# Optimization experiments

Hardware: AMD Instinct MI355X
Metric: run time of the kernel (lower is better)

Reference implementation:

```python
import jax, jax.numpy as jnp
import numpy as np

T_MAX = 26  # hardcoded 26 char steps in the torch module

def _resize(x, hw):
    # torch F.interpolate bilinear, align_corners=False (half-pixel) == jax linear, no antialias
    return jax.image.resize(x, x.shape[:-2] + hw, method='linear', antialias=False)

def _ce(logits, labels):
    # per-element cross entropy, labels int
    logp = jax.nn.log_softmax(logits, axis=-1)
    return -jnp.take_along_axis(logp, labels[:, None].astype(jnp.int32), axis=-1)[:, 0]


def setup_inputs() -> dict:
    key = jax.random.key(0)
    ks = jax.random.split(key, 6)
    b, H, W, L = 512, 32, 128, 64
    hm, wm, hl, wl = 16, 64, 8, 32
    return {
        'masks': jax.random.uniform(ks[0], (b, 1, H, W), dtype=jnp.float32),
        'backfore_feature': jax.random.normal(ks[1], (b, 2, H, W), dtype=jnp.float32),
        'seq1_attention_map': jax.random.uniform(ks[2], (b, L, T_MAX), dtype=jnp.float32),
        'char_middle': jax.random.normal(ks[3], (b, 27, hm, wm), dtype=jnp.float32),
        'char_low': jax.random.normal(ks[4], (b, 27, hl, wl), dtype=jnp.float32),
        'length': jax.random.randint(ks[5], (b,), 2, 27),
        'iteration': 1000,
        'alpha': jnp.float32(0.1),
    }


def reference(masks, backfore_feature, seq1_attention_map, char_middle, char_low, length, iteration, alpha):
    b, _, H, W = masks.shape
    f32 = masks.dtype
    masks_i = (masks > 0.5).astype(jnp.int32)                      # [b,1,H,W]
    sm = jax.nn.softmax(backfore_feature, axis=1)                  # [b,2,H,W]

    # ---- SegLoss: CE applied to softmax probs as if logits (faithful to torch) ----
    per_elem = _ce(sm.transpose(0, 2, 3, 1).reshape(-1, 2), masks_i.reshape(-1))
    if iteration > 20000:
        value = per_elem.reshape(b, -1).mean(1)
        sel = (value < 1.0).astype(f32)
        predmask_loss = (value * sel).sum() / jnp.maximum(sel.sum(), 1.0)
    else:
        predmask_loss = per_elem.mean()

    fore_mask = (sm[:, 1] > 0.5).astype(jnp.int32)[:, None]        # [b,1,H,W], int -> no grad
    Attn = jnp.transpose(seq1_attention_map, (0, 2, 1))            # [b,26,L]
    n = length - 1                                                  # valid chars per sample
    nf = n.astype(f32)
    row_valid = (jnp.arange(T_MAX)[None, :] < n[:, None]).astype(f32)  # [b,26]

    # ---- Correct_1D_Location (seg mask detached; Attn gets grads) ----
    fore_d = jax.lax.stop_gradient(fore_mask)
    interp = _resize(Attn[:, None], (T_MAX, W))[:, 0]              # [b,26,W]
    # pairwise sum_{i<j} sum_w (v_i v_j)^2 over the first n rows, vectorized
    sq = jnp.square(interp) * row_valid[:, :, None]
    S = sq.sum(1)
    S2 = jnp.square(sq).sum(1)
    irrelevant = (0.5 * (jnp.square(S) - S2).sum(-1) / nf).sum()
    act = jax.nn.sigmoid(70.0 * (interp - 0.1)) * row_valid[:, :, None]
    # sum_t act[t,w] * mask[h,w] == (sum_t act)[w] * mask[h,w]
    char_sum = jnp.clip(act.sum(1)[:, None, :] * fore_d[:, 0].astype(f32), 0.0, 1.0)  # [b,H,W]
    single2 = jnp.stack([1.0 - char_sum, char_sum], axis=-1)       # [b,H,W,2]
    correct_loss = _ce(single2.reshape(-1, 2), fore_d.reshape(-1)).mean() + irrelevant

    # ---- Char_Segmention_Loss (attention and fore mask detached) ----
    attn_clr = jax.lax.stop_gradient(Attn) * row_valid[:, :, None]  # clear_noise

    def char_branch(char_feat):
        h, w = char_feat.shape[2], char_feat.shape[3]
        fm = (_resize(fore_d.astype(f32), (h, w)) >= 0.4).astype(jnp.int32)   # [b,1,h,w]
        ai = _resize(attn_clr[:, None], (T_MAX, w))[:, 0]
        ab = (ai > alpha).astype(jnp.int32)                                   # [b,26,w]
        single = ab[:, :, None, :] * fm                                       # [b,26,h,w]
        mask27 = jnp.concatenate([1 - fm, single], axis=1)                    # [b,27,h,w]
        labels = jnp.argmax(mask27, axis=1).reshape(-1)
        cel = _ce(char_feat.transpose(0, 2, 3, 1).reshape(-1, 27), labels).mean()
        soft = jax.nn.softmax(char_feat, axis=1)
        m1 = soft[:, 1:].reshape(b, T_MAX, -1)
        m2 = mask27[:, 1:].astype(f32).reshape(b, T_MAX, -1)
        inter = (m1 * m2).sum(-1)
        score = (2.0 * inter + 1.0) / (m1.sum(-1) + m2.sum(-1) + 1.0)         # [b,26]
        dice = (((1.0 - score) * row_valid).sum(-1) / nf).sum() / b
        return cel + dice, mask27, soft

    loss_middle, _, soft_mid = char_branch(char_middle)
    loss_low, mask_low, soft_low = char_branch(char_low)

    return (predmask_loss, correct_loss, loss_low, loss_middle,
            mask_low, soft_mid[:, 1:], soft_low[:, 1:])
```

## Files before the change

### kernel.cpp

```cpp
#include <hip/hip_runtime.h>
#include <hip/hip_bf16.h>
#include <math.h>

#define NB 512
#define TT 26
#define LL 64
#define HH 32
#define WW 128

typedef unsigned long long ull;

__device__ __forceinline__ float wave_sum(float v) {
#pragma unroll
  for (int o = 32; o > 0; o >>= 1) v += __shfl_xor(v, o, 64);
  return v;
}

template<int CTRL, int RM>
__device__ __forceinline__ float dpp_add(float x) {
  int y = __builtin_amdgcn_update_dpp(0, __float_as_int(x), CTRL, RM, 0xf, true);
  return x + __int_as_float(y);
}
__device__ __forceinline__ float wave_red63(float x) {
  x = dpp_add<0x111, 0xf>(x);
  x = dpp_add<0x112, 0xf>(x);
  x = dpp_add<0x114, 0xf>(x);
  x = dpp_add<0x118, 0xf>(x);
  x = dpp_add<0x142, 0xa>(x);
  x = dpp_add<0x143, 0xc>(x);
  return x;
}

__global__ __launch_bounds__(128) void k_phase1(
    const float* __restrict__ seq, const int* __restrict__ length,
    const float* __restrict__ alpha_p, float* __restrict__ wsA,
    ull* __restrict__ amid, unsigned int* __restrict__ alow,
    float* __restrict__ irr_part)
{
  int b = blockIdx.x;
  int tid = threadIdx.x;
  __shared__ float att[LL * TT];
  __shared__ float wpart[2];
  const float* sb = seq + (size_t)b * (LL * TT);
  for (int i = tid; i < LL * TT; i += 128) att[i] = sb[i];
  __syncthreads();
  int n = length[b] - 1;
  float alpha = alpha_p[0];

  int w = tid;
  int k = w >> 1;
  int i0, i1; float c0, c1;
  if ((w & 1) == 0) {
    if (k == 0) { i0 = 0; i1 = 0; c0 = 1.f; c1 = 0.f; }
    else        { i0 = k - 1; i1 = k; c0 = 0.25f; c1 = 0.75f; }
  } else {
    if (k == 63) { i0 = 63; i1 = 63; c0 = 1.f; c1 = 0.f; }
    else         { i0 = k; i1 = k + 1; c0 = 0.75f; c1 = 0.25f; }
  }
  float S = 0.f, S2 = 0.f, A = 0.f;
  for (int t = 0; t < n; ++t) {
    float v = c0 * att[i0 * TT + t] + c1 * att[i1 * TT + t];
    float s = v * v;
    S += s; S2 += s * s;
    A += 1.f / (1.f + __expf(-70.f * (v - 0.1f)));
  }
  wsA[b * WW + w] = A;

  float c = S * S - S2;
  c = wave_sum(c);
  if ((tid & 63) == 0) wpart[tid >> 6] = c;
  __syncthreads();
  if (tid == 0) irr_part[b] = 0.5f * (wpart[0] + wpart[1]) / (float)n;

  if (tid < 64) {
    int x = tid;
    for (int t = 0; t < TT; ++t) {
      bool pred = (t < n) && (att[x * TT + t] > alpha);
      ull m = __ballot(pred);
      if (x == 0) amid[b * TT + t] = m;
    }
  } else {
    int x = tid - 64;
    for (int t = 0; t < TT; ++t) {
      bool pred = (x < 32) && (t < n) &&
                  (0.5f * (att[(2 * x) * TT + t] + att[(2 * x + 1) * TT + t]) > alpha);
      ull m = __ballot(pred);
      if (x == 0) alow[b * TT + t] = (unsigned int)m;
    }
  }
}

__global__ __launch_bounds__(256) void k_phase2(
    const float* __restrict__ masks, const float* __restrict__ bf,
    const float* __restrict__ wsA, float* __restrict__ seg_part,
    float* __restrict__ cor_part, ull* __restrict__ fmsk)
{
  int bid = blockIdx.x;
  int b = bid >> 2, q = bid & 3;
  int tid = threadIdx.x;
  int lane = tid & 63, wv = tid >> 6;
  const float* mb = masks + (size_t)b * 4096 + q * 1024;
  const float* fb = bf + (size_t)b * 8192 + q * 1024;

  float A = wsA[b * WW + (tid & 127)];
  float cs = fminf(fmaxf(A, 0.f), 1.f);
  float ce_fore = log1pf(__expf(1.f - 2.f * cs));

  float seg_acc = 0.f, cor_acc = 0.f;
  for (int k = 0; k < 4; ++k) {
    int px = k * 256 + tid;
    float m = mb[px];
    float b0 = fb[px];
    float b1 = fb[4096 + px];
    float mx = fmaxf(b0, b1);
    float e0 = __expf(b0 - mx), e1 = __expf(b1 - mx);
    float inv = 1.f / (e0 + e1);
    float p0 = e0 * inv, p1 = e1 * inv;
    float pm = fmaxf(p0, p1);
    float lse = pm + log1pf(__expf(-fabsf(p1 - p0)));
    seg_acc += lse - ((m > 0.5f) ? p1 : p0);
    bool fore = b1 > b0;
    cor_acc += fore ? ce_fore : 0.313261687518222834f;
    ull fbm = __ballot(fore);
    if (lane == 0) fmsk[(size_t)b * 64 + q * 16 + k * 4 + wv] = fbm;
  }
  seg_acc = wave_sum(seg_acc);
  cor_acc = wave_sum(cor_acc);
  __shared__ float ps[4], pc[4];
  if (lane == 0) { ps[wv] = seg_acc; pc[wv] = cor_acc; }
  __syncthreads();
  if (tid == 0) {
    seg_part[bid] = ps[0] + ps[1] + ps[2] + ps[3];
    cor_part[bid] = pc[0] + pc[1] + pc[2] + pc[3];
  }
}

__global__ __launch_bounds__(512) void k_chars(
    const float* __restrict__ cm, const float* __restrict__ cl,
    const ull* __restrict__ fmsk, const ull* __restrict__ amid,
    const unsigned int* __restrict__ alow,
    float* __restrict__ out_mask, float* __restrict__ out_smid,
    float* __restrict__ out_slow,
    float* __restrict__ celm_part, float* __restrict__ cell_part,
    float* __restrict__ inter_midP, float* __restrict__ m1s_midP, float* __restrict__ m2s_midP,
    float* __restrict__ inter_low, float* __restrict__ m1s_low, float* __restrict__ m2s_low)
{
  int blk = blockIdx.x;
  int tid = threadIdx.x;
  int lane = tid & 63, wv = tid >> 6;

  __shared__ float s_red_in[8][TT], s_red_m1[8][TT], s_ce[8];

  if (blk >= 256) {
    int bm_ = blk - 256;
    int b = bm_ >> 1, h = bm_ & 1;
    int ly = tid >> 6;
    int x = tid & 63;
    int px = h * 512 + tid;
    __shared__ ull s_bits[TT];
    __shared__ unsigned s_cols[64];
    __shared__ ull s_fmw[32];
    __shared__ ull s_fmrow[8];
    if (tid < TT) s_bits[tid] = amid[b * TT + tid];
    if (tid >= 32 && tid < 64) s_fmw[tid - 32] = fmsk[(size_t)b * 64 + h * 32 + (tid - 32)];
    __syncthreads();
    if (tid < 64) {
      unsigned cb = 0;
#pragma unroll
      for (int t = 0; t < TT; ++t) cb |= (unsigned)((s_bits[t] >> tid) & 1ULL) << t;
      s_cols[tid] = cb;
    }
    __syncthreads();

    int word = x >> 5;
    int p = (x & 31) * 2;
    ull r0 = s_fmw[4 * ly + word];
    ull r1 = s_fmw[4 * ly + 2 + word];
    int cnt = (int)((r0 >> p) & 1) + (int)((r0 >> (p + 1)) & 1)
            + (int)((r1 >> p) & 1) + (int)((r1 >> (p + 1)) & 1);
    bool fm = cnt >= 2;
    unsigned cbk = s_cols[x];
    int lab = (fm && cbk) ? __ffs((int)cbk) : 0;
    if (!fm) cbk = 0;
    ull bm = __ballot(fm);
    if (lane == 0) s_fmrow[wv] = bm;

    const float* base = cm + (size_t)b * 27 * 1024 + px;
    float v[27];
    float xl = 0.f, s0 = 0.f;
#pragma unroll
    for (int c = 0; c < 27; ++c) {
      float r = base[(size_t)c * 1024];
      xl = (c == lab) ? r : xl;
      r = __expf(r);
      v[c] = r;
      s0 += r;
    }
    float inv0 = 1.f / s0;
    float ce_part = __logf(s0) - xl;

    float* os = out_smid + (size_t)b * 26 * 1024 + px;
#pragma unroll
    for (int t = 0; t < TT; ++t) {
      float m1 = v[t + 1] * inv0;
      os[(size_t)t * 1024] = m1;
      float ri = wave_red63(((cbk >> t) & 1) ? m1 : 0.f);
      float rm = wave_red63(m1);
      if (lane == 63) { s_red_in[wv][t] = ri; s_red_m1[wv][t] = rm; }
    }
    float rce = wave_red63(ce_part);
    if (lane == 63) s_ce[wv] = rce;
    __syncthreads();
    if (tid < TT) {
      float m2v = 0.f;
#pragma unroll
      for (int r = 0; r < 8; ++r) m2v += (float)__popcll(s_fmrow[r] & s_bits[tid]);
      float si = 0.f, sm = 0.f;
#pragma unroll
      for (int w = 0; w < 8; ++w) { si += s_red_in[w][tid]; sm += s_red_m1[w][tid]; }
      int o = (2 * b + h) * TT + tid;
      m2s_midP[o] = m2v;
      inter_midP[o] = si;
      m1s_midP[o] = sm;
    }
    if (tid == TT) {
      float c8 = 0.f;
#pragma unroll
      for (int w = 0; w < 8; ++w) c8 += s_ce[w];
      celm_part[2 * b + h] = c8;
    }
  } else {
    int blkL = blk;
    int bI = tid >> 8;
    int bb = blkL * 2 + bI;
    int px = tid & 255;
    int y = px >> 5, x = px & 31;
    __shared__ unsigned l_bits[2][TT];
    __shared__ unsigned s_colsL[2][32];
    __shared__ ull s_fmwL[2][64];
    __shared__ unsigned s_fmrow32[2][8];
    if (tid < 2 * TT) {
      int bi = tid / TT, t = tid - bi * TT;
      l_bits[bi][t] = alow[(blkL * 2 + bi) * TT + t];
    }
    if (tid >= 128 && tid < 256) {
      int j = tid - 128;
      s_fmwL[j >> 6][j & 63] = fmsk[(size_t)(blkL * 2 + (j >> 6)) * 64 + (j & 63)];
    }
    __syncthreads();
    if (tid < 64) {
      int bi = tid >> 5, xc = tid & 31;
      unsigned cb = 0;
#pragma unroll
      for (int t = 0; t < TT; ++t) cb |= ((l_bits[bi][t] >> xc) & 1u) << t;
      s_colsL[bi][xc] = cb;
    }
    __syncthreads();

    int wb = 4 * x + 1;
    int word = wb >> 6;
    int p = wb & 63;
    ull r0 = s_fmwL[bI][(4 * y + 1) * 2 + word];
    ull r1 = s_fmwL[bI][(4 * y + 2) * 2 + word];
    int cnt = (int)((r0 >> p) & 1) + (int)((r0 >> (p + 1)) & 1)
            + (int)((r1 >> p) & 1) + (int)((r1 >> (p + 1)) & 1);
    bool fm = cnt >= 2;
    unsigned cbk = s_colsL[bI][x];
    int lab = (fm && cbk) ? __ffs((int)cbk) : 0;
    if (!fm) cbk = 0;
    ull bm = __ballot(fm);
    if (lane == 0) {
      int wq = wv & 3;
      s_fmrow32[bI][2 * wq] = (unsigned)bm;
      s_fmrow32[bI][2 * wq + 1] = (unsigned)(bm >> 32);
    }

    const float* base = cl + (size_t)bb * 27 * 256 + px;
    float v[27];
    float xl = 0.f, s0 = 0.f;
#pragma unroll
    for (int c = 0; c < 27; ++c) {
      float r = base[(size_t)c * 256];
      xl = (c == lab) ? r : xl;
      r = __expf(r);
      v[c] = r;
      s0 += r;
    }
    float inv0 = 1.f / s0;
    float ce_part = __logf(s0) - xl;

    float* om  = out_mask + (size_t)bb * 27 * 256 + px;
    float* osf = out_slow + (size_t)bb * 26 * 256 + px;
    om[0] = fm ? 0.f : 1.f;
#pragma unroll
    for (int t = 0; t < TT; ++t) {
      float m1 = v[t + 1] * inv0;
      osf[(size_t)t * 256] = m1;
      bool m2 = (cbk >> t) & 1;
      om[(size_t)(t + 1) * 256] = m2 ? 1.f : 0.f;
      float ri = wave_red63(m2 ? m1 : 0.f);
      float rm = wave_red63(m1);
      if (lane == 63) { s_red_in[wv][t] = ri; s_red_m1[wv][t] = rm; }
    }
    float rce = wave_red63(ce_part);
    if (lane == 63) s_ce[wv] = rce;
    __syncthreads();
    if (tid < 2 * TT) {
      int bi = tid / TT, t = tid - bi * TT;
      float m2v = 0.f;
#pragma unroll
      for (int r = 0; r < 8; ++r) m2v += (float)__popc(s_fmrow32[bi][r] & l_bits[bi][t]);
      float si = 0.f, sm = 0.f;
#pragma unroll
      for (int w = 0; w < 4; ++w) { si += s_red_in[bi * 4 + w][t]; sm += s_red_m1[bi * 4 + w][t]; }
      int o = (blkL * 2 + bi) * TT + t;
      m2s_low[o] = m2v;
      inter_low[o] = si;
      m1s_low[o] = sm;
    }
    if (tid >= 2 * TT && tid < 2 * TT + 2) {
      int bi = tid - 2 * TT;
      cell_part[blkL * 2 + bi] = s_ce[bi * 4] + s_ce[bi * 4 + 1] + s_ce[bi * 4 + 2] + s_ce[bi * 4 + 3];
    }
  }
}

__global__ __launch_bounds__(1024) void k_final(
    const float* __restrict__ seg_part, const float* __restrict__ cor_part,
    const float* __restrict__ irr_part, const float* __restrict__ celm_part,
    const float* __restrict__ cell_part,
    const float* __restrict__ inter_midP, const float* __restrict__ m1s_midP,
    const float* __restrict__ m2s_midP,
    const float* __restrict__ inter_low, const float* __restrict__ m1s_low,
    const float* __restrict__ m2s_low,
    const int* __restrict__ length, const int* __restrict__ iter_p,
    float* __restrict__ out)
{
  int tid = threadIdx.x;
  float dm = 0.f, dl = 0.f;
  for (int i = tid; i < NB * TT; i += 1024) {
    int b = i / TT, t = i - b * TT;
    int n = length[b] - 1;
    if (t < n) {
      float inv_n = 1.f / (float)n;
      int o0 = (2 * b) * TT + t, o1 = (2 * b + 1) * TT + t;
      float im = inter_midP[o0] + inter_midP[o1];
      float mm = m1s_midP[o0] + m1s_midP[o1];
      float m2 = m2s_midP[o0] + m2s_midP[o1];
      dm += (1.f - (2.f * im + 1.f) / (mm + m2 + 1.f)) * inv_n;
      dl += (1.f - (2.f * inter_low[i] + 1.f) / (m1s_low[i] + m2s_low[i] + 1.f)) * inv_n;
    }
  }
  float ss = 0.f, sel = 0.f, ssel = 0.f;
  float irr = 0.f, cell = 0.f;
  for (int b = tid; b < NB; b += 1024) {
    float v = seg_part[4 * b] + seg_part[4 * b + 1] + seg_part[4 * b + 2] + seg_part[4 * b + 3];
    ss += v;
    float val = v * (1.f / 4096.f);
    if (val < 1.f) { sel += 1.f; ssel += val; }
    irr += irr_part[b]; cell += cell_part[b];
  }
  float cor = 0.f, celm = 0.f;
  for (int i = tid; i < 4 * NB; i += 1024) cor += cor_part[i];
  for (int i = tid; i < 2 * NB; i += 1024) celm += celm_part[i];

  dm = wave_sum(dm); dl = wave_sum(dl); ss = wave_sum(ss);
  sel = wave_sum(sel); ssel = wave_sum(ssel);
  irr = wave_sum(irr); celm = wave_sum(celm); cell = wave_sum(cell);
  cor = wave_sum(cor);
  __shared__ float red[9][16];
  int wv = tid >> 6;
  if ((tid & 63) == 0) {
    red[0][wv] = dm; red[1][wv] = dl; red[2][wv] = ss; red[3][wv] = sel;
    red[4][wv] = ssel; red[5][wv] = irr; red[6][wv] = celm; red[7][wv] = cell;
    red[8][wv] = cor;
  }
  __syncthreads();
  if (tid == 0) {
    float a[9];
#pragma unroll
    for (int j = 0; j < 9; ++j) {
      float s = 0.f;
      for (int i = 0; i < 16; ++i) s += red[j][i];
      a[j] = s;
    }
    float pred = (iter_p[0] > 20000) ? (a[4] / fmaxf(a[3], 1.f)) : (a[2] / 2097152.f);
    out[0] = pred;
    out[1] = a[8] / 2097152.f + a[5];
    out[2] = a[7] / 131072.f + a[1] / 512.f;
    out[3] = a[6] / 524288.f + a[0] / 512.f;
  }
}

extern "C" void kernel_launch(void* const* d_in, const int* in_sizes, int n_in,
                              void* d_out, int out_size, void* d_ws, size_t ws_size,
                              hipStream_t stream) {
  (void)in_sizes; (void)n_in; (void)out_size; (void)ws_size;
  const float* masks  = (const float*)d_in[0];
  const float* bf     = (const float*)d_in[1];
  const float* seq    = (const float*)d_in[2];
  const float* cmid   = (const float*)d_in[3];
  const float* clow   = (const float*)d_in[4];
  const int*   length = (const int*)d_in[5];
  const int*   iter   = (const int*)d_in[6];
  const float* alpha  = (const float*)d_in[7];
  float* out = (float*)d_out;

  char* ws = (char*)d_ws;
  float* seg_part   = (float*)(ws + 0);
  float* cor_part   = (float*)(ws + 8192);
  float* irr_part   = (float*)(ws + 16384);
  float* celm_part  = (float*)(ws + 18432);
  float* cell_part  = (float*)(ws + 22528);
  float* inter_midP = (float*)(ws + 24576);
  float* m1s_midP   = (float*)(ws + 131072);
  float* m2s_midP   = (float*)(ws + 237568);
  ull*          amid = (ull*)(ws + 344064);
  unsigned int* alow = (unsigned int*)(ws + 450560);
  ull*          fmsk = (ull*)(ws + 503808);
  float*        wsA  = (float*)(ws + 765952);
  float* inter_low = (float*)(ws + 765952);
  float* m1s_low   = (float*)(ws + 819200);
  float* m2s_low   = (float*)(ws + 872448);

  k_phase1<<<NB, 128, 0, stream>>>(seq, length, alpha, wsA, amid, alow, irr_part);
  k_phase2<<<NB * 4, 256, 0, stream>>>(masks, bf, wsA, seg_part, cor_part, fmsk);

  float* out_mask = out + 4;
  float* out_smid = out + 4 + 3538944;
  float* out_slow = out + 4 + 3538944 + 13631488;

  k_chars<<<256 + 2 * NB, 512, 0, stream>>>(cmid, clow, fmsk, amid, alow,
                                            out_mask, out_smid, out_slow,
                                            celm_part, cell_part,
                                            inter_midP, m1s_midP, m2s_midP,
                                            inter_low, m1s_low, m2s_low);
  k_final<<<1, 1024, 0, stream>>>(seg_part, cor_part, irr_part, celm_part, cell_part,
                                  inter_midP, m1s_midP, m2s_midP,
                                  inter_low, m1s_low, m2s_low, length, iter, out);
}
```

Baseline: 68.55 us.

## Replace per-step wave DPP reductions with fp16 shared-memory transposed reductions

In k_chars, the 26 pairs of wave-wide DPP reductions per pixel (intersection and softmax sum) are replaced. Each thread now stores its softmax values as fp16 in shared memory, along with its char-bit column mask. After a barrier, threads are reassigned so each one sums a 32-pixel chunk for one time step, using vectorized uint4 loads, and the chunk partials are then combined. This cuts the long serial DPP chains but adds about 34 KB of shared memory per block, which may lower occupancy, and it reduces the precision of the dice sums by accumulating from fp16 values.

Result: no change. 69.02 us (+0.7%).

```diff
diff --git a/kernel.cpp b/kernel.cpp
--- a/kernel.cpp
+++ b/kernel.cpp
@@ -1,5 +1,5 @@
 #include <hip/hip_runtime.h>
-#include <hip/hip_bf16.h>
+#include <hip/hip_fp16.h>
 #include <math.h>
 
 #define NB 512
@@ -29,6 +29,15 @@
   x = dpp_add<0x142, 0xa>(x);
   x = dpp_add<0x143, 0xc>(x);
   return x;
+}
+
+__device__ __forceinline__ void unpack_acc(unsigned hpair, unsigned c0, unsigned c1,
+                                           int t, float& msum, float& isum) {
+  __half2 h2 = *reinterpret_cast<__half2*>(&hpair);
+  float2 f = __half22float2(h2);
+  msum += f.x + f.y;
+  isum += ((c0 >> t) & 1) ? f.x : 0.f;
+  isum += ((c1 >> t) & 1) ? f.y : 0.f;
 }
 
 __global__ __launch_bounds__(128) void k_phase1(
@@ -148,30 +157,35 @@
   int blk = blockIdx.x;
   int tid = threadIdx.x;
   int lane = tid & 63, wv = tid >> 6;
-
-  __shared__ float s_red_in[8][TT], s_red_m1[8][TT], s_ce[8];
+  __shared__ __align__(16) char smem[34432];
 
   if (blk >= 256) {
     int bm_ = blk - 256;
     int b = bm_ >> 1, h = bm_ & 1;
+    __half*   m1h     = (__half*)(smem);
+    unsigned* cbkA    = (unsigned*)(smem + 27040);
+    float (*part_in)[16] = (float(*)[16])(smem + 29088);
+    float (*part_m1)[16] = (float(*)[16])(smem + 30752);
+    ull*      s_bits  = (ull*)(smem + 32416);
+    unsigned* s_cols  = (unsigned*)(smem + 32624);
+    ull*      s_fmw   = (ull*)(smem + 32880);
+    ull*      s_fmrow = (ull*)(smem + 33136);
+    float*    s_ce    = (float*)(smem + 33200);
+
+    if (tid < TT) s_bits[tid] = amid[b * TT + tid];
+    if (tid >= 32 && tid < 64) s_fmw[tid - 32] = fmsk[(size_t)b * 64 + h * 32 + (tid - 32)];
+    __syncthreads();
+    if (tid < 64) {
+      unsigned cb = 0;
+#pragma unroll
+      for (int t = 0; t < TT; ++t) cb |= (unsigned)((s_bits[t] >> tid) & 1ULL) << t;
+      s_cols[tid] = cb;
+    }
+    __syncthreads();
+
     int ly = tid >> 6;
     int x = tid & 63;
     int px = h * 512 + tid;
-    __shared__ ull s_bits[TT];
-    __shared__ unsigned s_cols[64];
-    __shared__ ull s_fmw[32];
-    __shared__ ull s_fmrow[8];
-    if (tid < TT) s_bits[tid] = amid[b * TT + tid];
-    if (tid >= 32 && tid < 64) s_fmw[tid - 32] = fmsk[(size_t)b * 64 + h * 32 + (tid - 32)];
-    __syncthreads();
-    if (tid < 64) {
-      unsigned cb = 0;
-#pragma unroll
-      for (int t = 0; t < TT; ++t) cb |= (unsigned)((s_bits[t] >> tid) & 1ULL) << t;
-      s_cols[tid] = cb;
-    }
-    __syncthreads();
-
     int word = x >> 5;
     int p = (x & 31) * 2;
     ull r0 = s_fmw[4 * ly + word];
@@ -182,8 +196,9 @@
     unsigned cbk = s_cols[x];
     int lab = (fm && cbk) ? __ffs((int)cbk) : 0;
     if (!fm) cbk = 0;
-    ull bm = __ballot(fm);
-    if (lane == 0) s_fmrow[wv] = bm;
+    ull bmv = __ballot(fm);
+    if (lane == 0) s_fmrow[wv] = bmv;
+    cbkA[tid] = cbk;
 
     const float* base = cm + (size_t)b * 27 * 1024 + px;
     float v[27];
@@ -204,20 +219,40 @@
     for (int t = 0; t < TT; ++t) {
       float m1 = v[t + 1] * inv0;
       os[(size_t)t * 1024] = m1;
-      float ri = wave_red63(((cbk >> t) & 1) ? m1 : 0.f);
-      float rm = wave_red63(m1);
-      if (lane == 63) { s_red_in[wv][t] = ri; s_red_m1[wv][t] = rm; }
+      m1h[t * 520 + tid] = __float2half(m1);
     }
     float rce = wave_red63(ce_part);
     if (lane == 63) s_ce[wv] = rce;
     __syncthreads();
+
+    {
+      int t = tid >> 4, c = tid & 15;
+      if (t < TT) {
+        const uint4* pm = (const uint4*)(m1h + t * 520 + c * 32);
+        const uint4* pc = (const uint4*)(cbkA + c * 32);
+        float isum = 0.f, msum = 0.f;
+#pragma unroll
+        for (int q = 0; q < 4; ++q) {
+          uint4 mh = pm[q];
+          uint4 cA = pc[2 * q];
+          uint4 cB = pc[2 * q + 1];
+          unpack_acc(mh.x, cA.x, cA.y, t, msum, isum);
+          unpack_acc(mh.y, cA.z, cA.w, t, msum, isum);
+          unpack_acc(mh.z, cB.x, cB.y, t, msum, isum);
+          unpack_acc(mh.w, cB.z, cB.w, t, msum, isum);
+        }
+        part_in[t][c] = isum;
+        part_m1[t][c] = msum;
+      }
+    }
+    __syncthreads();
     if (tid < TT) {
       float m2v = 0.f;
 #pragma unroll
       for (int r = 0; r < 8; ++r) m2v += (float)__popcll(s_fmrow[r] & s_bits[tid]);
       float si = 0.f, sm = 0.f;
 #pragma unroll
-      for (int w = 0; w < 8; ++w) { si += s_red_in[w][tid]; sm += s_red_m1[w][tid]; }
+      for (int c = 0; c < 16; ++c) { si += part_in[tid][c]; sm += part_m1[tid][c]; }
       int o = (2 * b + h) * TT + tid;
       m2s_midP[o] = m2v;
       inter_midP[o] = si;
@@ -230,50 +265,56 @@
       celm_part[2 * b + h] = c8;
     }
   } else {
-    int blkL = blk;
+    __half*   m1hL    = (__half*)(smem);
+    unsigned* cbkL    = (unsigned*)(smem + 27456);
+    float (*partL_in)[8] = (float(*)[8])(smem + 29504);
+    float (*partL_m1)[8] = (float(*)[8])(smem + 31168);
+    unsigned* l_bits  = (unsigned*)(smem + 32832);
+    unsigned* colsL   = (unsigned*)(smem + 33040);
+    ull*      fmwL    = (ull*)(smem + 33296);
+    unsigned* fmrow32 = (unsigned*)(smem + 34320);
+    float*    ceL     = (float*)(smem + 34384);
+
     int bI = tid >> 8;
-    int bb = blkL * 2 + bI;
+    int bb = blk * 2 + bI;
     int px = tid & 255;
     int y = px >> 5, x = px & 31;
-    __shared__ unsigned l_bits[2][TT];
-    __shared__ unsigned s_colsL[2][32];
-    __shared__ ull s_fmwL[2][64];
-    __shared__ unsigned s_fmrow32[2][8];
     if (tid < 2 * TT) {
       int bi = tid / TT, t = tid - bi * TT;
-      l_bits[bi][t] = alow[(blkL * 2 + bi) * TT + t];
+      l_bits[bi * TT + t] = alow[(blk * 2 + bi) * TT + t];
     }
     if (tid >= 128 && tid < 256) {
       int j = tid - 128;
-      s_fmwL[j >> 6][j & 63] = fmsk[(size_t)(blkL * 2 + (j >> 6)) * 64 + (j & 63)];
+      fmwL[j] = fmsk[(size_t)(blk * 2 + (j >> 6)) * 64 + (j & 63)];
     }
     __syncthreads();
     if (tid < 64) {
       int bi = tid >> 5, xc = tid & 31;
       unsigned cb = 0;
 #pragma unroll
-      for (int t = 0; t < TT; ++t) cb |= ((l_bits[bi][t] >> xc) & 1u) << t;
-      s_colsL[bi][xc] = cb;
+      for (int t = 0; t < TT; ++t) cb |= ((l_bits[bi * TT + t] >> xc) & 1u) << t;
+      colsL[bi * 32 + xc] = cb;
     }
     __syncthreads();
 
     int wb = 4 * x + 1;
     int word = wb >> 6;
     int p = wb & 63;
-    ull r0 = s_fmwL[bI][(4 * y + 1) * 2 + word];
-    ull r1 = s_fmwL[bI][(4 * y + 2) * 2 + word];
+    ull r0 = fmwL[bI * 64 + (4 * y + 1) * 2 + word];
+    ull r1 = fmwL[bI * 64 + (4 * y + 2) * 2 + word];
     int cnt = (int)((r0 >> p) & 1) + (int)((r0 >> (p + 1)) & 1)
             + (int)((r1 >> p) & 1) + (int)((r1 >> (p + 1)) & 1);
     bool fm = cnt >= 2;
-    unsigned cbk = s_colsL[bI][x];
+    unsigned cbk = colsL[bI * 32 + x];
     int lab = (fm && cbk) ? __ffs((int)cbk) : 0;
     if (!fm) cbk = 0;
-    ull bm = __ballot(fm);
+    ull bmv = __ballot(fm);
     if (lane == 0) {
       int wq = wv & 3;
-      s_fmrow32[bI][2 * wq] = (unsigned)bm;
-      s_fmrow32[bI][2 * wq + 1] = (unsigned)(bm >> 32);
-    }
+      fmrow32[bI * 8 + 2 * wq] = (unsigned)bmv;
+      fmrow32[bI * 8 + 2 * wq + 1] = (unsigned)(bmv >> 32);
+    }
+    cbkL[bI * 256 + px] = cbk;
 
     const float* base = cl + (size_t)bb * 27 * 256 + px;
     float v[27];
@@ -296,31 +337,51 @@
     for (int t = 0; t < TT; ++t) {
       float m1 = v[t + 1] * inv0;
       osf[(size_t)t * 256] = m1;
-      bool m2 = (cbk >> t) & 1;
-      om[(size_t)(t + 1) * 256] = m2 ? 1.f : 0.f;
-      float ri = wave_red63(m2 ? m1 : 0.f);
-      float rm = wave_red63(m1);
-      if (lane == 63) { s_red_in[wv][t] = ri; s_red_m1[wv][t] = rm; }
+      om[(size_t)(t + 1) * 256] = ((cbk >> t) & 1) ? 1.f : 0.f;
+      m1hL[(bI * TT + t) * 264 + px] = __float2half(m1);
     }
     float rce = wave_red63(ce_part);
-    if (lane == 63) s_ce[wv] = rce;
+    if (lane == 63) ceL[wv] = rce;
+    __syncthreads();
+
+    {
+      int r = tid & 255;
+      int t = r >> 3, c = r & 7;
+      if (t < TT) {
+        const uint4* pm = (const uint4*)(m1hL + (bI * TT + t) * 264 + c * 32);
+        const uint4* pc = (const uint4*)(cbkL + bI * 256 + c * 32);
+        float isum = 0.f, msum = 0.f;
+#pragma unroll
+        for (int q = 0; q < 4; ++q) {
+          uint4 mh = pm[q];
+          uint4 cA = pc[2 * q];
+          uint4 cB = pc[2 * q + 1];
+          unpack_acc(mh.x, cA.x, cA.y, t, msum, isum);
+          unpack_acc(mh.y, cA.z, cA.w, t, msum, isum);
+          unpack_acc(mh.z, cB.x, cB.y, t, msum, isum);
+          unpack_acc(mh.w, cB.z, cB.w, t, msum, isum);
+        }
+        partL_in[bI * TT + t][c] = isum;
+        partL_m1[bI * TT + t][c] = msum;
+      }
+    }
     __syncthreads();
     if (tid < 2 * TT) {
       int bi = tid / TT, t = tid - bi * TT;
       float m2v = 0.f;
 #pragma unroll
-      for (int r = 0; r < 8; ++r) m2v += (float)__popc(s_fmrow32[bi][r] & l_bits[bi][t]);
+      for (int yy = 0; yy < 8; ++yy) m2v += (float)__popc(fmrow32[bi * 8 + yy] & l_bits[bi * TT + t]);
       float si = 0.f, sm = 0.f;
 #pragma unroll
-      for (int w = 0; w < 4; ++w) { si += s_red_in[bi * 4 + w][t]; sm += s_red_m1[bi * 4 + w][t]; }
-      int o = (blkL * 2 + bi) * TT + t;
+      for (int c = 0; c < 8; ++c) { si += partL_in[bi * TT + t][c]; sm += partL_m1[bi * TT + t][c]; }
+      int o = (blk * 2 + bi) * TT + t;
       m2s_low[o] = m2v;
       inter_low[o] = si;
       m1s_low[o] = sm;
     }
     if (tid >= 2 * TT && tid < 2 * TT + 2) {
       int bi = tid - 2 * TT;
-      cell_part[blkL * 2 + bi] = s_ce[bi * 4] + s_ce[bi * 4 + 1] + s_ce[bi * 4 + 2] + s_ce[bi * 4 + 3];
+      cell_part[blk * 2 + bi] = ceL[bi * 4] + ceL[bi * 4 + 1] + ceL[bi * 4 + 2] + ceL[bi * 4 + 3];
     }
   }
 }
```

## Fuse phase1, phase2 and char kernels into one per-sample megakernel

Applied to the files above, without the earlier changes.

Merges the three producer kernels into a single 1024-thread block per sample. Attention bitmasks, foreground masks and the sigmoid accumulators now stay in LDS instead of going through global workspace, and two kernel launches are removed. The cost is lower parallelism and occupancy. Only 512 large blocks run, the low-res branch uses just 256 of the 1024 threads, and there are serial phases with block-wide syncs, so memory-bound work may overlap less well.

Measured after the change: 65.63 us. 4.3% less time.

```diff
diff --git a/kernel.cpp b/kernel.cpp
--- a/kernel.cpp
+++ b/kernel.cpp
@@ -1,5 +1,4 @@
 #include <hip/hip_runtime.h>
-#include <hip/hip_bf16.h>
 #include <math.h>
 
 #define NB 512
@@ -31,161 +30,153 @@
   return x;
 }
 
-__global__ __launch_bounds__(128) void k_phase1(
-    const float* __restrict__ seq, const int* __restrict__ length,
-    const float* __restrict__ alpha_p, float* __restrict__ wsA,
-    ull* __restrict__ amid, unsigned int* __restrict__ alow,
-    float* __restrict__ irr_part)
+__global__ __launch_bounds__(1024) void k_mega(
+    const float* __restrict__ masks, const float* __restrict__ bf,
+    const float* __restrict__ seq, const float* __restrict__ cm,
+    const float* __restrict__ cl, const int* __restrict__ length,
+    const float* __restrict__ alpha_p,
+    float* __restrict__ out_mask, float* __restrict__ out_smid,
+    float* __restrict__ out_slow,
+    float* __restrict__ seg_part, float* __restrict__ cor_part,
+    float* __restrict__ irr_part, float* __restrict__ celm_part,
+    float* __restrict__ cell_part,
+    float* __restrict__ inter_mid, float* __restrict__ m1s_mid, float* __restrict__ m2s_mid,
+    float* __restrict__ inter_low, float* __restrict__ m1s_low, float* __restrict__ m2s_low)
 {
   int b = blockIdx.x;
   int tid = threadIdx.x;
+  int lane = tid & 63, wv = tid >> 6;
+
   __shared__ float att[LL * TT];
+  __shared__ float wsA_lds[WW];
+  __shared__ ull s_bits[TT];
+  __shared__ unsigned s_alow[TT];
+  __shared__ unsigned s_cols_mid[64];
+  __shared__ unsigned s_cols_low[32];
+  __shared__ ull fmsk_lds[64];
+  __shared__ ull s_fmrow[16];
+  __shared__ unsigned fmrow32[8];
+  __shared__ float s_red_in[16][TT], s_red_m1[16][TT];
+  __shared__ float s_ce[16];
+  __shared__ float ps[16], pc[16];
   __shared__ float wpart[2];
-  const float* sb = seq + (size_t)b * (LL * TT);
-  for (int i = tid; i < LL * TT; i += 128) att[i] = sb[i];
-  __syncthreads();
+
   int n = length[b] - 1;
   float alpha = alpha_p[0];
 
-  int w = tid;
-  int k = w >> 1;
-  int i0, i1; float c0, c1;
-  if ((w & 1) == 0) {
-    if (k == 0) { i0 = 0; i1 = 0; c0 = 1.f; c1 = 0.f; }
-    else        { i0 = k - 1; i1 = k; c0 = 0.25f; c1 = 0.75f; }
-  } else {
-    if (k == 63) { i0 = 63; i1 = 63; c0 = 1.f; c1 = 0.f; }
-    else         { i0 = k; i1 = k + 1; c0 = 0.75f; c1 = 0.25f; }
-  }
-  float S = 0.f, S2 = 0.f, A = 0.f;
-  for (int t = 0; t < n; ++t) {
-    float v = c0 * att[i0 * TT + t] + c1 * att[i1 * TT + t];
-    float s = v * v;
-    S += s; S2 += s * s;
-    A += 1.f / (1.f + __expf(-70.f * (v - 0.1f)));
-  }
-  wsA[b * WW + w] = A;
-
-  float c = S * S - S2;
-  c = wave_sum(c);
-  if ((tid & 63) == 0) wpart[tid >> 6] = c;
-  __syncthreads();
-  if (tid == 0) irr_part[b] = 0.5f * (wpart[0] + wpart[1]) / (float)n;
-
+  const float* sb = seq + (size_t)b * (LL * TT);
+  for (int i = tid; i < LL * TT; i += 1024) att[i] = sb[i];
+  __syncthreads();
+
+  if (tid < 128) {
+    int w = tid;
+    int k = w >> 1;
+    int i0, i1; float c0, c1;
+    if ((w & 1) == 0) {
+      if (k == 0) { i0 = 0; i1 = 0; c0 = 1.f; c1 = 0.f; }
+      else        { i0 = k - 1; i1 = k; c0 = 0.25f; c1 = 0.75f; }
+    } else {
+      if (k == 63) { i0 = 63; i1 = 63; c0 = 1.f; c1 = 0.f; }
+      else         { i0 = k; i1 = k + 1; c0 = 0.75f; c1 = 0.25f; }
+    }
+    float S = 0.f, S2 = 0.f, A = 0.f;
+    for (int t = 0; t < n; ++t) {
+      float v = c0 * att[i0 * TT + t] + c1 * att[i1 * TT + t];
+      float s = v * v;
+      S += s; S2 += s * s;
+      A += 1.f / (1.f + __expf(-70.f * (v - 0.1f)));
+    }
+    wsA_lds[w] = A;
+    float c = S * S - S2;
+    c = wave_sum(c);
+    if (lane == 0) wpart[wv] = c;
+  }
   if (tid < 64) {
     int x = tid;
     for (int t = 0; t < TT; ++t) {
       bool pred = (t < n) && (att[x * TT + t] > alpha);
       ull m = __ballot(pred);
-      if (x == 0) amid[b * TT + t] = m;
-    }
-  } else {
+      if (x == 0) s_bits[t] = m;
+    }
+  } else if (tid < 128) {
     int x = tid - 64;
     for (int t = 0; t < TT; ++t) {
       bool pred = (x < 32) && (t < n) &&
                   (0.5f * (att[(2 * x) * TT + t] + att[(2 * x + 1) * TT + t]) > alpha);
       ull m = __ballot(pred);
-      if (x == 0) alow[b * TT + t] = (unsigned int)m;
-    }
-  }
-}
-
-__global__ __launch_bounds__(256) void k_phase2(
-    const float* __restrict__ masks, const float* __restrict__ bf,
-    const float* __restrict__ wsA, float* __restrict__ seg_part,
-    float* __restrict__ cor_part, ull* __restrict__ fmsk)
-{
-  int bid = blockIdx.x;
-  int b = bid >> 2, q = bid & 3;
-  int tid = threadIdx.x;
-  int lane = tid & 63, wv = tid >> 6;
-  const float* mb = masks + (size_t)b * 4096 + q * 1024;
-  const float* fb = bf + (size_t)b * 8192 + q * 1024;
-
-  float A = wsA[b * WW + (tid & 127)];
-  float cs = fminf(fmaxf(A, 0.f), 1.f);
-  float ce_fore = log1pf(__expf(1.f - 2.f * cs));
-
-  float seg_acc = 0.f, cor_acc = 0.f;
-  for (int k = 0; k < 4; ++k) {
-    int px = k * 256 + tid;
-    float m = mb[px];
-    float b0 = fb[px];
-    float b1 = fb[4096 + px];
-    float mx = fmaxf(b0, b1);
-    float e0 = __expf(b0 - mx), e1 = __expf(b1 - mx);
-    float inv = 1.f / (e0 + e1);
-    float p0 = e0 * inv, p1 = e1 * inv;
-    float pm = fmaxf(p0, p1);
-    float lse = pm + log1pf(__expf(-fabsf(p1 - p0)));
-    seg_acc += lse - ((m > 0.5f) ? p1 : p0);
-    bool fore = b1 > b0;
-    cor_acc += fore ? ce_fore : 0.313261687518222834f;
-    ull fbm = __ballot(fore);
-    if (lane == 0) fmsk[(size_t)b * 64 + q * 16 + k * 4 + wv] = fbm;
-  }
-  seg_acc = wave_sum(seg_acc);
-  cor_acc = wave_sum(cor_acc);
-  __shared__ float ps[4], pc[4];
-  if (lane == 0) { ps[wv] = seg_acc; pc[wv] = cor_acc; }
+      if (x == 0) s_alow[t] = (unsigned)m;
+    }
+  }
+  __syncthreads();
+  if (tid == 0) irr_part[b] = 0.5f * (wpart[0] + wpart[1]) / (float)n;
+
+  if (tid < 64) {
+    unsigned cb = 0;
+#pragma unroll
+    for (int t = 0; t < TT; ++t) cb |= (unsigned)((s_bits[t] >> tid) & 1ULL) << t;
+    s_cols_mid[tid] = cb;
+  } else if (tid < 96) {
+    int xc = tid - 64;
+    unsigned cb = 0;
+#pragma unroll
+    for (int t = 0; t < TT; ++t) cb |= ((s_alow[t] >> xc) & 1u) << t;
+    s_cols_low[xc] = cb;
+  }
+
+  {
+    const float* mb = masks + (size_t)b * 4096;
+    const float* fb = bf + (size_t)b * 8192;
+    float A = wsA_lds[tid & 127];
+    float cs = fminf(fmaxf(A, 0.f), 1.f);
+    float ce_fore = log1pf(__expf(1.f - 2.f * cs));
+    float seg_acc = 0.f, cor_acc = 0.f;
+    for (int k = 0; k < 4; ++k) {
+      int px = k * 1024 + tid;
+      float m = mb[px];
+      float b0 = fb[px];
+      float b1 = fb[4096 + px];
+      float mx = fmaxf(b0, b1);
+      float e0 = __expf(b0 - mx), e1 = __expf(b1 - mx);
+      float inv = 1.f / (e0 + e1);
+      float p0 = e0 * inv, p1 = e1 * inv;
+      float pm = fmaxf(p0, p1);
+      float lse = pm + log1pf(__expf(-fabsf(p1 - p0)));
+      seg_acc += lse - ((m > 0.5f) ? p1 : p0);
+      bool fore = b1 > b0;
+      cor_acc += fore ? ce_fore : 0.313261687518222834f;
+      ull fbm = __ballot(fore);
+      if (lane == 0) fmsk_lds[k * 16 + wv] = fbm;
+    }
+    seg_acc = wave_red63(seg_acc);
+    cor_acc = wave_red63(cor_acc);
+    if (lane == 63) { ps[wv] = seg_acc; pc[wv] = cor_acc; }
+  }
   __syncthreads();
   if (tid == 0) {
-    seg_part[bid] = ps[0] + ps[1] + ps[2] + ps[3];
-    cor_part[bid] = pc[0] + pc[1] + pc[2] + pc[3];
-  }
-}
-
-__global__ __launch_bounds__(512) void k_chars(
-    const float* __restrict__ cm, const float* __restrict__ cl,
-    const ull* __restrict__ fmsk, const ull* __restrict__ amid,
-    const unsigned int* __restrict__ alow,
-    float* __restrict__ out_mask, float* __restrict__ out_smid,
-    float* __restrict__ out_slow,
-    float* __restrict__ celm_part, float* __restrict__ cell_part,
-    float* __restrict__ inter_midP, float* __restrict__ m1s_midP, float* __restrict__ m2s_midP,
-    float* __restrict__ inter_low, float* __restrict__ m1s_low, float* __restrict__ m2s_low)
-{
-  int blk = blockIdx.x;
-  int tid = threadIdx.x;
-  int lane = tid & 63, wv = tid >> 6;
-
-  __shared__ float s_red_in[8][TT], s_red_m1[8][TT], s_ce[8];
-
-  if (blk >= 256) {
-    int bm_ = blk - 256;
-    int b = bm_ >> 1, h = bm_ & 1;
-    int ly = tid >> 6;
+    float s = 0.f, c = 0.f;
+#pragma unroll
+    for (int i = 0; i < 16; ++i) { s += ps[i]; c += pc[i]; }
+    seg_part[b] = s;
+    cor_part[b] = c;
+  }
+
+  {
+    int y = wv;
     int x = tid & 63;
-    int px = h * 512 + tid;
-    __shared__ ull s_bits[TT];
-    __shared__ unsigned s_cols[64];
-    __shared__ ull s_fmw[32];
-    __shared__ ull s_fmrow[8];
-    if (tid < TT) s_bits[tid] = amid[b * TT + tid];
-    if (tid >= 32 && tid < 64) s_fmw[tid - 32] = fmsk[(size_t)b * 64 + h * 32 + (tid - 32)];
-    __syncthreads();
-    if (tid < 64) {
-      unsigned cb = 0;
-#pragma unroll
-      for (int t = 0; t < TT; ++t) cb |= (unsigned)((s_bits[t] >> tid) & 1ULL) << t;
-      s_cols[tid] = cb;
-    }
-    __syncthreads();
-
     int word = x >> 5;
     int p = (x & 31) * 2;
-    ull r0 = s_fmw[4 * ly + word];
-    ull r1 = s_fmw[4 * ly + 2 + word];
+    ull r0 = fmsk_lds[4 * y + word];
+    ull r1 = fmsk_lds[4 * y + 2 + word];
     int cnt = (int)((r0 >> p) & 1) + (int)((r0 >> (p + 1)) & 1)
             + (int)((r1 >> p) & 1) + (int)((r1 >> (p + 1)) & 1);
     bool fm = cnt >= 2;
-    unsigned cbk = s_cols[x];
+    unsigned cbk = s_cols_mid[x];
     int lab = (fm && cbk) ? __ffs((int)cbk) : 0;
     if (!fm) cbk = 0;
-    ull bm = __ballot(fm);
-    if (lane == 0) s_fmrow[wv] = bm;
-
-    const float* base = cm + (size_t)b * 27 * 1024 + px;
+    ull bmv = __ballot(fm);
+    if (lane == 0) s_fmrow[wv] = bmv;
+
+    const float* base = cm + (size_t)b * 27 * 1024 + tid;
     float v[27];
     float xl = 0.f, s0 = 0.f;
 #pragma unroll
@@ -199,7 +190,7 @@
     float inv0 = 1.f / s0;
     float ce_part = __logf(s0) - xl;
 
-    float* os = out_smid + (size_t)b * 26 * 1024 + px;
+    float* os = out_smid + (size_t)b * 26 * 1024 + tid;
 #pragma unroll
     for (int t = 0; t < TT; ++t) {
       float m1 = v[t + 1] * inv0;
@@ -210,72 +201,49 @@
     }
     float rce = wave_red63(ce_part);
     if (lane == 63) s_ce[wv] = rce;
-    __syncthreads();
-    if (tid < TT) {
-      float m2v = 0.f;
-#pragma unroll
-      for (int r = 0; r < 8; ++r) m2v += (float)__popcll(s_fmrow[r] & s_bits[tid]);
-      float si = 0.f, sm = 0.f;
-#pragma unroll
-      for (int w = 0; w < 8; ++w) { si += s_red_in[w][tid]; sm += s_red_m1[w][tid]; }
-      int o = (2 * b + h) * TT + tid;
-      m2s_midP[o] = m2v;
-      inter_midP[o] = si;
-      m1s_midP[o] = sm;
-    }
-    if (tid == TT) {
-      float c8 = 0.f;
-#pragma unroll
-      for (int w = 0; w < 8; ++w) c8 += s_ce[w];
-      celm_part[2 * b + h] = c8;
-    }
-  } else {
-    int blkL = blk;
-    int bI = tid >> 8;
-    int bb = blkL * 2 + bI;
-    int px = tid & 255;
+  }
+  __syncthreads();
+  if (tid < TT) {
+    float m2v = 0.f;
+#pragma unroll
+    for (int r = 0; r < 16; ++r) m2v += (float)__popcll(s_fmrow[r] & s_bits[tid]);
+    float si = 0.f, sm = 0.f;
+#pragma unroll
+    for (int w = 0; w < 16; ++w) { si += s_red_in[w][tid]; sm += s_red_m1[w][tid]; }
+    int o = b * TT + tid;
+    m2s_mid[o] = m2v;
+    inter_mid[o] = si;
+    m1s_mid[o] = sm;
+  }
+  if (tid == TT) {
+    float c16 = 0.f;
+#pragma unroll
+    for (int w = 0; w < 16; ++w) c16 += s_ce[w];
+    celm_part[b] = c16;
+  }
+  __syncthreads();
+
+  if (tid < 256) {
+    int px = tid;
     int y = px >> 5, x = px & 31;
-    __shared__ unsigned l_bits[2][TT];
-    __shared__ unsigned s_colsL[2][32];
-    __shared__ ull s_fmwL[2][64];
-    __shared__ unsigned s_fmrow32[2][8];
-    if (tid < 2 * TT) {
-      int bi = tid / TT, t = tid - bi * TT;
-      l_bits[bi][t] = alow[(blkL * 2 + bi) * TT + t];
-    }
-    if (tid >= 128 && tid < 256) {
-      int j = tid - 128;
-      s_fmwL[j >> 6][j & 63] = fmsk[(size_t)(blkL * 2 + (j >> 6)) * 64 + (j & 63)];
-    }
-    __syncthreads();
-    if (tid < 64) {
-      int bi = tid >> 5, xc = tid & 31;
-      unsigned cb = 0;
-#pragma unroll
-      for (int t = 0; t < TT; ++t) cb |= ((l_bits[bi][t] >> xc) & 1u) << t;
-      s_colsL[bi][xc] = cb;
-    }
-    __syncthreads();
-
     int wb = 4 * x + 1;
     int word = wb >> 6;
     int p = wb & 63;
-    ull r0 = s_fmwL[bI][(4 * y + 1) * 2 + word];
-    ull r1 = s_fmwL[bI][(4 * y + 2) * 2 + word];
+    ull r0 = fmsk_lds[(4 * y + 1) * 2 + word];
+    ull r1 = fmsk_lds[(4 * y + 2) * 2 + word];
     int cnt = (int)((r0 >> p) & 1) + (int)((r0 >> (p + 1)) & 1)
             + (int)((r1 >> p) & 1) + (int)((r1 >> (p + 1)) & 1);
     bool fm = cnt >= 2;
-    unsigned cbk = s_colsL[bI][x];
+    unsigned cbk = s_cols_low[x];
     int lab = (fm && cbk) ? __ffs((int)cbk) : 0;
     if (!fm) cbk = 0;
-    ull bm = __ballot(fm);
+    ull bmv = __ballot(fm);
     if (lane == 0) {
-      int wq = wv & 3;
-      s_fmrow32[bI][2 * wq] = (unsigned)bm;
-      s_fmrow32[bI][2 * wq + 1] = (unsigned)(bm >> 32);
-    }
-
-    const float* base = cl + (size_t)bb * 27 * 256 + px;
+      fmrow32[2 * wv] = (unsigned)bmv;
+      fmrow32[2 * wv + 1] = (unsigned)(bmv >> 32);
+    }
+
+    const float* base = cl + (size_t)b * 27 * 256 + px;
     float v[27];
     float xl = 0.f, s0 = 0.f;
 #pragma unroll
@@ -289,8 +257,8 @@
     float inv0 = 1.f / s0;
     float ce_part = __logf(s0) - xl;
 
-    float* om  = out_mask + (size_t)bb * 27 * 256 + px;
-    float* osf = out_slow + (size_t)bb * 26 * 256 + px;
+    float* om  = out_mask + (size_t)b * 27 * 256 + px;
+    float* osf = out_slow + (size_t)b * 26 * 256 + px;
     om[0] = fm ? 0.f : 1.f;
 #pragma unroll
     for (int t = 0; t < TT; ++t) {
@@ -304,33 +272,29 @@
     }
     float rce = wave_red63(ce_part);
     if (lane == 63) s_ce[wv] = rce;
-    __syncthreads();
-    if (tid < 2 * TT) {
-      int bi = tid / TT, t = tid - bi * TT;
-      float m2v = 0.f;
-#pragma unroll
-      for (int r = 0; r < 8; ++r) m2v += (float)__popc(s_fmrow32[bi][r] & l_bits[bi][t]);
-      float si = 0.f, sm = 0.f;
-#pragma unroll
-      for (int w = 0; w < 4; ++w) { si += s_red_in[bi * 4 + w][t]; sm += s_red_m1[bi * 4 + w][t]; }
-      int o = (blkL * 2 + bi) * TT + t;
-      m2s_low[o] = m2v;
-      inter_low[o] = si;
-      m1s_low[o] = sm;
-    }
-    if (tid >= 2 * TT && tid < 2 * TT + 2) {
-      int bi = tid - 2 * TT;
-      cell_part[blkL * 2 + bi] = s_ce[bi * 4] + s_ce[bi * 4 + 1] + s_ce[bi * 4 + 2] + s_ce[bi * 4 + 3];
-    }
-  }
+  }
+  __syncthreads();
+  if (tid < TT) {
+    float m2v = 0.f;
+#pragma unroll
+    for (int yy = 0; yy < 8; ++yy) m2v += (float)__popc(fmrow32[yy] & s_alow[tid]);
+    float si = 0.f, sm = 0.f;
+#pragma unroll
+    for (int w = 0; w < 4; ++w) { si += s_red_in[w][tid]; sm += s_red_m1[w][tid]; }
+    int o = b * TT + tid;
+    m2s_low[o] = m2v;
+    inter_low[o] = si;
+    m1s_low[o] = sm;
+  }
+  if (tid == TT) cell_part[b] = s_ce[0] + s_ce[1] + s_ce[2] + s_ce[3];
 }
 
 __global__ __launch_bounds__(1024) void k_final(
     const float* __restrict__ seg_part, const float* __restrict__ cor_part,
     const float* __restrict__ irr_part, const float* __restrict__ celm_part,
     const float* __restrict__ cell_part,
-    const float* __restrict__ inter_midP, const float* __restrict__ m1s_midP,
-    const float* __restrict__ m2s_midP,
+    const float* __restrict__ inter_mid, const float* __restrict__ m1s_mid,
+    const float* __restrict__ m2s_mid,
     const float* __restrict__ inter_low, const float* __restrict__ m1s_low,
     const float* __restrict__ m2s_low,
     const int* __restrict__ length, const int* __restrict__ iter_p,
@@ -343,26 +307,19 @@
     int n = length[b] - 1;
     if (t < n) {
       float inv_n = 1.f / (float)n;
-      int o0 = (2 * b) * TT + t, o1 = (2 * b + 1) * TT + t;
-      float im = inter_midP[o0] + inter_midP[o1];
-      float mm = m1s_midP[o0] + m1s_midP[o1];
-      float m2 = m2s_midP[o0] + m2s_midP[o1];
-      dm += (1.f - (2.f * im + 1.f) / (mm + m2 + 1.f)) * inv_n;
+      dm += (1.f - (2.f * inter_mid[i] + 1.f) / (m1s_mid[i] + m2s_mid[i] + 1.f)) * inv_n;
       dl += (1.f - (2.f * inter_low[i] + 1.f) / (m1s_low[i] + m2s_low[i] + 1.f)) * inv_n;
     }
   }
   float ss = 0.f, sel = 0.f, ssel = 0.f;
-  float irr = 0.f, cell = 0.f;
+  float irr = 0.f, cell = 0.f, celm = 0.f, cor = 0.f;
   for (int b = tid; b < NB; b += 1024) {
-    float v = seg_part[4 * b] + seg_part[4 * b + 1] + seg_part[4 * b + 2] + seg_part[4 * b + 3];
+    float v = seg_part[b];
     ss += v;
     float val = v * (1.f / 4096.f);
     if (val < 1.f) { sel += 1.f; ssel += val; }
-    irr += irr_part[b]; cell += cell_part[b];
-  }
-  float cor = 0.f, celm = 0.f;
-  for (int i = tid; i < 4 * NB; i += 1024) cor += cor_part[i];
-  for (int i = tid; i < 2 * NB; i += 1024) celm += celm_part[i];
+    irr += irr_part[b]; cell += cell_part[b]; celm += celm_part[b]; cor += cor_part[b];
+  }
 
   dm = wave_sum(dm); dl = wave_sum(dl); ss = wave_sum(ss);
   sel = wave_sum(sel); ssel = wave_sum(ssel);
@@ -407,35 +364,28 @@
   float* out = (float*)d_out;
 
   char* ws = (char*)d_ws;
-  float* seg_part   = (float*)(ws + 0);
-  float* cor_part   = (float*)(ws + 8192);
-  float* irr_part   = (float*)(ws + 16384);
-  float* celm_part  = (float*)(ws + 18432);
-  float* cell_part  = (float*)(ws + 22528);
-  float* inter_midP = (float*)(ws + 24576);
-  float* m1s_midP   = (float*)(ws + 131072);
-  float* m2s_midP   = (float*)(ws + 237568);
-  ull*          amid = (ull*)(ws + 344064);
-  unsigned int* alow = (unsigned int*)(ws + 450560);
-  ull*          fmsk = (ull*)(ws + 503808);
-  float*        wsA  = (float*)(ws + 765952);
-  float* inter_low = (float*)(ws + 765952);
-  float* m1s_low   = (float*)(ws + 819200);
-  float* m2s_low   = (float*)(ws + 872448);
-
-  k_phase1<<<NB, 128, 0, stream>>>(seq, length, alpha, wsA, amid, alow, irr_part);
-  k_phase2<<<NB * 4, 256, 0, stream>>>(masks, bf, wsA, seg_part, cor_part, fmsk);
+  float* seg_part  = (float*)(ws + 0);
+  float* cor_part  = (float*)(ws + 2048);
+  float* irr_part  = (float*)(ws + 4096);
+  float* celm_part = (float*)(ws + 6144);
+  float* cell_part = (float*)(ws + 8192);
+  float* inter_mid = (float*)(ws + 10240);
+  float* m1s_mid   = (float*)(ws + 63488);
+  float* m2s_mid   = (float*)(ws + 116736);
+  float* inter_low = (float*)(ws + 169984);
+  float* m1s_low   = (float*)(ws + 223232);
+  float* m2s_low   = (float*)(ws + 276480);
 
   float* out_mask = out + 4;
   float* out_smid = out + 4 + 3538944;
   float* out_slow = out + 4 + 3538944 + 13631488;
 
-  k_chars<<<256 + 2 * NB, 512, 0, stream>>>(cmid, clow, fmsk, amid, alow,
-                                            out_mask, out_smid, out_slow,
-                                            celm_part, cell_part,
-                                            inter_midP, m1s_midP, m2s_midP,
-                                            inter_low, m1s_low, m2s_low);
+  k_mega<<<NB, 1024, 0, stream>>>(masks, bf, seq, cmid, clow, length, alpha,
+                                  out_mask, out_smid, out_slow,
+                                  seg_part, cor_part, irr_part, celm_part, cell_part,
+                                  inter_mid, m1s_mid, m2s_mid,
+                                  inter_low, m1s_low, m2s_low);
   k_final<<<1, 1024, 0, stream>>>(seg_part, cor_part, irr_part, celm_part, cell_part,
-                                  inter_midP, m1s_midP, m2s_midP,
+                                  inter_mid, m1s_mid, m2s_mid,
                                   inter_low, m1s_low, m2s_low, length, iter, out);
 }
```
